# Performance work log

Hardware: AMD Instinct MI355X
Metric: run time of the kernel (lower is better)

Reference implementation:

```python
import jax, jax.numpy as jnp
import numpy as np

B, T, C, H = 2, 2048, 1024, 16
D = C // H  # head dim = 64


def setup_inputs() -> dict:
    key = jax.random.key(0)
    k1, k2, k3 = jax.random.split(key, 3)
    x = jax.random.normal(k1, (B, T, C), dtype=jnp.float32)
    w_attn = jax.random.normal(k2, (C, 3 * C), dtype=jnp.float32) * (1.0 / np.sqrt(C))
    b_attn = jnp.zeros((3 * C,), dtype=jnp.float32)
    w_proj = jax.random.normal(k3, (C, C), dtype=jnp.float32) * (1.0 / np.sqrt(C))
    b_proj = jnp.zeros((C,), dtype=jnp.float32)
    return {"x": x, "w_attn": w_attn, "b_attn": b_attn, "w_proj": w_proj, "b_proj": b_proj}


def reference(x, w_attn, b_attn, w_proj, b_proj):
    Bx, Tx, Cx = x.shape
    qkv = x @ w_attn + b_attn  # [B, T, 3C]
    q, k, v = jnp.split(qkv, 3, axis=-1)
    # [B, H, T, D]
    q = q.reshape(Bx, Tx, H, D).swapaxes(1, 2)
    k = k.reshape(Bx, Tx, H, D).swapaxes(1, 2)
    v = v.reshape(Bx, Tx, H, D).swapaxes(1, 2)
    scale = 1.0 / jnp.sqrt(jnp.float32(D))
    att = jnp.einsum('bhqd,bhkd->bhqk', q, k) * scale  # [B, H, T, T]
    causal = jnp.tril(jnp.ones((Tx, Tx), dtype=bool))
    att = jnp.where(causal[None, None], att, -jnp.inf)
    att = jax.nn.softmax(att, axis=-1)
    y = jnp.einsum('bhqk,bhkd->bhqd', att, v)  # [B, H, T, D]
    y = y.swapaxes(1, 2).reshape(Bx, Tx, Cx)
    return y @ w_proj + b_proj
```

## Files before the change

### kernel.cpp

```cpp
#include <hip/hip_runtime.h>
#include <hip/hip_bf16.h>


typedef __attribute__((ext_vector_type(8))) short short8x;
typedef __attribute__((ext_vector_type(4))) float float4x;
typedef __attribute__((ext_vector_type(4))) unsigned short ushort4x;
typedef __attribute__((ext_vector_type(2))) unsigned int uint2x;

#define MFMA_BF16 __builtin_amdgcn_mfma_f32_16x16x32_bf16

typedef const __attribute__((address_space(1))) void gvoid_t;
typedef __attribute__((address_space(3))) void lvoid_t;
#define GLOAD_LDS16(g, l) __builtin_amdgcn_global_load_lds((gvoid_t*)(g), (lvoid_t*)(l), 16, 0, 0)

__device__ __forceinline__ unsigned short f2b(float f) {
    unsigned int u = __float_as_uint(f);
    u = (u + 0x7FFFu + ((u >> 16) & 1u)) >> 16;
    return (unsigned short)u;
}
__device__ __forceinline__ unsigned int pk2(float a, float b) {
    return __builtin_amdgcn_perm(__float_as_uint(b) + 0x8000u,
                                 __float_as_uint(a) + 0x8000u, 0x07060302u);
}
__device__ __forceinline__ unsigned int pk2t(float a, float b) {
    return __builtin_amdgcn_perm(__float_as_uint(b),
                                 __float_as_uint(a), 0x07060302u);
}

__device__ __forceinline__ void stage32(const unsigned short* g, size_t rs,
                                        short* ldst, int w0, int lane) {
    const int r8 = lane >> 3;
    const int sc = ((lane & 7) ^ r8) * 8;
#pragma unroll
    for (int q = 0; q < 4; q++) {
        GLOAD_LDS16(g + (size_t)(w0 + q * 8 + r8) * rs + sc,
                    ldst + (w0 + q * 8) * 64);
    }
}

__global__ __launch_bounds__(256) void prep(const float* __restrict__ x,
                                            unsigned short* __restrict__ xb,
                                            const float* __restrict__ wa,
                                            unsigned short* __restrict__ waT,
                                            const float* __restrict__ wp,
                                            unsigned short* __restrict__ wpT) {
    __shared__ float tile[32][33];
    const int blk = blockIdx.x;
    if (blk < 4096) {
        int i = blk * 256 + threadIdx.x;
        float4 v = ((const float4*)x)[i];
        ushort4x o = { f2b(v.x), f2b(v.y), f2b(v.z), f2b(v.w) };
        ((ushort4x*)xb)[i] = o;
        return;
    }
    int idx = blk - 4096;
    int bx = idx & 127;
    int by = idx >> 7;
    const float* in;
    unsigned short* outp;
    int cols;
    if (bx < 96) { in = wa; outp = waT; cols = 3072; }
    else         { in = wp; outp = wpT; cols = 1024; bx -= 96; }
    const int tx = threadIdx.x & 31, ty = threadIdx.x >> 5;
    const int cbase = bx * 32, rbase = by * 32;
    int c = cbase + tx;
    for (int j = 0; j < 32; j += 8)
        tile[ty + j][tx] = in[(size_t)(rbase + ty + j) * cols + c];
    __syncthreads();
    int rr = rbase + tx;
    for (int j = 0; j < 32; j += 8) {
        int cc = cbase + ty + j;
        outp[(size_t)cc * 1024 + rr] = f2b(tile[tx][ty + j]);
    }
}

template <bool SWAP>
__device__ __forceinline__ void qkv_mainloop(const unsigned short* Ag,
                                             const unsigned short* Bg,
                                             short* lA, short* lB,
                                             float4x (&acc)[4][4],
                                             int wave, int lane, int wr, int wc,
                                             int quad, int l16, int sw) {
    const int K = 1024;
    for (int kk = 0; kk < K; kk += 64) {
        stage32(Ag + kk, K, lA, wave * 32, lane);
        stage32(Bg + kk, K, lB, wave * 32, lane);
        __syncthreads();

#pragma unroll
        for (int kk2 = 0; kk2 < 2; kk2++) {
            short8x a[4], b[4];
#pragma unroll
            for (int i = 0; i < 4; i++)
                a[i] = *(const short8x*)&lA[(wr * 64 + i * 16 + l16) * 64 +
                                            ((kk2 * 4 + quad) ^ sw) * 8];
#pragma unroll
            for (int j = 0; j < 4; j++)
                b[j] = *(const short8x*)&lB[(wc * 64 + j * 16 + l16) * 64 +
                                            ((kk2 * 4 + quad) ^ sw) * 8];
#pragma unroll
            for (int i = 0; i < 4; i++)
#pragma unroll
                for (int j = 0; j < 4; j++)
                    acc[i][j] = SWAP ? MFMA_BF16(b[j], a[i], acc[i][j], 0, 0, 0)
                                     : MFMA_BF16(a[i], b[j], acc[i][j], 0, 0, 0);
        }
        __syncthreads();
    }
}

__global__ __launch_bounds__(256, 4) void gemm_qkv(const unsigned short* __restrict__ A,
                                                   const unsigned short* __restrict__ BT,
                                                   const float* __restrict__ bias,
                                                   unsigned short* __restrict__ QK,
                                                   unsigned short* __restrict__ VTg) {
    __shared__ union {
        struct { short A[128 * 64]; short B[128 * 64]; } s;
        short vt[4][64 * 80];
    } lds;

    const int K = 1024;
    const int lane = threadIdx.x & 63;
    const int wave = threadIdx.x >> 6;
    const int quad = lane >> 4;
    const int l16  = lane & 15;
    const int sw   = l16 & 7;

    const int rblk = blockIdx.y * 128;
    const int cblk = blockIdx.x * 128;
    const int wr = wave >> 1, wc = wave & 1;
    const bool qk = (blockIdx.x < 16);

    float4x acc[4][4] = {};

    const unsigned short* Ag = A  + (size_t)rblk * K;
    const unsigned short* Bg = BT + (size_t)cblk * K;

    if (qk) qkv_mainloop<true >(Ag, Bg, lds.s.A, lds.s.B, acc, wave, lane, wr, wc, quad, l16, sw);
    else    qkv_mainloop<false>(Ag, Bg, lds.s.A, lds.s.B, acc, wave, lane, wr, wc, quad, l16, sw);

    const int rbase = rblk + wr * 64;
    const int cbase = cblk + wc * 64;

    if (qk) {
        const float sc = (blockIdx.x < 8) ? 0.18033688f : 1.0f;
#pragma unroll
        for (int i = 0; i < 4; i++) {
            const int r = rbase + i * 16 + l16;
#pragma unroll
            for (int j = 0; j < 4; j++) {
                const int c = cbase + j * 16 + quad * 4;
                float4 bv = *(const float4*)&bias[c];
                uint2x p = { pk2((acc[i][j][0] + bv.x) * sc, (acc[i][j][1] + bv.y) * sc),
                             pk2((acc[i][j][2] + bv.z) * sc, (acc[i][j][3] + bv.w) * sc) };
                *(uint2x*)&QK[(size_t)r * 2048 + c] = p;
            }
        }
    } else {
#pragma unroll
        for (int i = 0; i < 4; i++) {
#pragma unroll
            for (int j = 0; j < 4; j++) {
                int c = cbase + j * 16 + l16;
                float bv = bias[c];
                uint2x p = { pk2(acc[i][j][0] + bv, acc[i][j][1] + bv),
                             pk2(acc[i][j][2] + bv, acc[i][j][3] + bv) };
                *(uint2x*)&lds.vt[wave][(j * 16 + l16) * 80 + i * 16 + quad * 4] = p;
            }
        }
        const int h   = (cbase - 2048) >> 6;
        const int hb  = (rbase >> 11) * 16 + h;
        const int tb0 = rbase & 2047;
#pragma unroll
        for (int p = 0; p < 8; p++) {
            int dd   = p * 8 + (lane >> 3);
            int toff = (lane & 7) * 8;
            short8x vv = *(const short8x*)&lds.vt[wave][dd * 80 + toff];
            *(short8x*)&VTg[((size_t)(hb * 64 + dd)) * 2048 + tb0 + toff] = vv;
        }
    }
}

__global__ __launch_bounds__(256) void gemm_proj(const unsigned short* __restrict__ A,
                                                 const unsigned short* __restrict__ BT,
                                                 const float* __restrict__ bias,
                                                 float* __restrict__ out) {
    __shared__ struct { short A[64 * 64]; short B[128 * 64]; } lds;

    const int K = 1024, N = 1024;
    const int lane = threadIdx.x & 63;
    const int wave = threadIdx.x >> 6;
    const int quad = lane >> 4;
    const int l16  = lane & 15;
    const int sw   = l16 & 7;

    const int rblk = blockIdx.y * 64;
    const int cblk = blockIdx.x * 128;

    float4x acc[4][2] = {};

    const unsigned short* Ag = A  + (size_t)rblk * K;
    const unsigned short* Bg = BT + (size_t)cblk * K;

    for (int kk = 0; kk < K; kk += 64) {
        if (wave < 2) {
            stage32(Ag + kk, K, lds.A, wave * 32, lane);
        } else {
            stage32(Bg + kk, K, lds.B, (wave - 2) * 64, lane);
            stage32(Bg + kk, K, lds.B, (wave - 2) * 64 + 32, lane);
        }
        __syncthreads();

#pragma unroll
        for (int kk2 = 0; kk2 < 2; kk2++) {
            short8x b[2];
#pragma unroll
            for (int j = 0; j < 2; j++)
                b[j] = *(const short8x*)&lds.B[(wave * 32 + j * 16 + l16) * 64 +
                                               ((kk2 * 4 + quad) ^ sw) * 8];
#pragma unroll
            for (int i = 0; i < 4; i++) {
                short8x a = *(const short8x*)&lds.A[(i * 16 + l16) * 64 +
                                                    ((kk2 * 4 + quad) ^ sw) * 8];
#pragma unroll
                for (int j = 0; j < 2; j++)
                    acc[i][j] = MFMA_BF16(a, b[j], acc[i][j], 0, 0, 0);
            }
        }
        __syncthreads();
    }

#pragma unroll
    for (int j = 0; j < 2; j++) {
        const int c = cblk + wave * 32 + j * 16 + l16;
        const float bv = bias[c];
#pragma unroll
        for (int i = 0; i < 4; i++) {
#pragma unroll
            for (int reg = 0; reg < 4; reg++) {
                int r = rblk + i * 16 + quad * 4 + reg;
                out[(size_t)r * N + c] = acc[i][j][reg] + bv;
            }
        }
    }
}

__global__ __launch_bounds__(256) void attn_kernel(const unsigned short* __restrict__ QK,
                                                   const unsigned short* __restrict__ VT,
                                                   unsigned short* __restrict__ Y) {
    __shared__ __attribute__((aligned(16))) short Kl[2][64 * 64];
    __shared__ __attribute__((aligned(16))) short Vl[2][64 * 64];
    __shared__ __attribute__((aligned(16))) short Pl[4][2048];

    const int tid  = threadIdx.x;
    const int lane = tid & 63;
    const int wave = tid >> 6;
    const int quad = lane >> 4;
    const int l16  = lane & 15;
    const int sw   = l16 & 7;

    const int bid = blockIdx.x;
    const int qb  = 31 - (bid >> 5);
    const int bh  = bid & 31;
    const int b = bh >> 4, h = bh & 15;

    const unsigned short* Qp = QK + ((size_t)b * 2048) * 2048 + h * 64;
    const unsigned short* Kp = Qp + 1024;
    const unsigned short* Vp = VT + (size_t)bh * 64 * 2048;

    const int qbase = qb * 64 + wave * 16;
    const int ntb   = qb + 1;

    short8x aq[2];
#pragma unroll
    for (int kk = 0; kk < 2; kk++)
        aq[kk] = *(const short8x*)(Qp + (size_t)(qbase + l16) * 2048 + kk * 32 + quad * 8);

    const short ONE = (short)0x3F80;
    const short8x ones = { ONE, ONE, ONE, ONE, ONE, ONE, ONE, ONE };

    if (wave < 2) stage32(Kp, 2048, Kl[0], wave * 32, lane);
    else          stage32(Vp, 2048, Vl[0], (wave - 2) * 32, lane);
    __syncthreads();

    float4x lacc = {};
    float4x O[4] = {};

    for (int it = 0; it < ntb; it++) {
        const int kb = it * 64;
        const short* Kc = Kl[it & 1];
        const short* Vc = Vl[it & 1];

        if (it + 1 < ntb) {
            const int kb2 = kb + 64;
            if (wave < 2) stage32(Kp + (size_t)kb2 * 2048, 2048, Kl[(it + 1) & 1], wave * 32, lane);
            else          stage32(Vp + kb2, 2048, Vl[(it + 1) & 1], (wave - 2) * 32, lane);
        }

        float4x S[4];
#pragma unroll
        for (int t = 0; t < 4; t++) {
            short8x kf0 = *(const short8x*)&Kc[(t * 16 + l16) * 64 + ((quad) ^ sw) * 8];
            short8x kf1 = *(const short8x*)&Kc[(t * 16 + l16) * 64 + ((4 + quad) ^ sw) * 8];
            S[t] = (float4x){0.f, 0.f, 0.f, 0.f};
            S[t] = MFMA_BF16(kf0, aq[0], S[t], 0, 0, 0);
            S[t] = MFMA_BF16(kf1, aq[1], S[t], 0, 0, 0);
        }

        if (kb + 64 > qbase) {
            int q = qbase + l16;
#pragma unroll
            for (int t = 0; t < 4; t++)
#pragma unroll
                for (int reg = 0; reg < 4; reg++)
                    if (kb + t * 16 + quad * 4 + reg > q) S[t][reg] = -1e38f;
        }

#pragma unroll
        for (int t = 0; t < 4; t++) {
            float e0 = __builtin_amdgcn_exp2f(S[t][0]);
            float e1 = __builtin_amdgcn_exp2f(S[t][1]);
            float e2 = __builtin_amdgcn_exp2f(S[t][2]);
            float e3 = __builtin_amdgcn_exp2f(S[t][3]);
            uint2x p = { pk2t(e0, e1), pk2t(e2, e3) };
            *(uint2x*)&Pl[wave][l16 * 64 + ((2 * t + (quad >> 1)) ^ sw) * 8 + (quad & 1) * 4] = p;
        }

#pragma unroll
        for (int kc = 0; kc < 2; kc++) {
            short8x bp = *(const short8x*)&Pl[wave][l16 * 64 + ((4 * kc + quad) ^ sw) * 8];
            lacc = MFMA_BF16(ones, bp, lacc, 0, 0, 0);
#pragma unroll
            for (int dt = 0; dt < 4; dt++) {
                short8x vf = *(const short8x*)&Vc[(dt * 16 + l16) * 64 + ((kc * 4 + quad) ^ sw) * 8];
                O[dt] = MFMA_BF16(vf, bp, O[dt], 0, 0, 0);
            }
        }
        __syncthreads();
    }

    float rl = 1.0f / lacc[0];
#pragma unroll
    for (int dt = 0; dt < 4; dt++) {
        uint2x o = { pk2(O[dt][0] * rl, O[dt][1] * rl),
                     pk2(O[dt][2] * rl, O[dt][3] * rl) };
        *(uint2x*)&Pl[wave][l16 * 64 + ((2 * dt + (quad >> 1)) ^ sw) * 8 + (quad & 1) * 4] = o;
    }
    const int t = qbase + l16;
#pragma unroll
    for (int cc = 0; cc < 2; cc++) {
        short8x row = *(const short8x*)&Pl[wave][l16 * 64 + ((2 * quad + cc) ^ sw) * 8];
        *(short8x*)&Y[((size_t)(b * 2048 + t)) * 1024 + h * 64 + (2 * quad + cc) * 8] = row;
    }
}

extern "C" void kernel_launch(void* const* d_in, const int* in_sizes, int n_in,
                              void* d_out, int out_size, void* d_ws, size_t ws_size,
                              hipStream_t stream) {
    const float* x      = (const float*)d_in[0];
    const float* w_attn = (const float*)d_in[1];
    const float* b_attn = (const float*)d_in[2];
    const float* w_proj = (const float*)d_in[3];
    const float* b_proj = (const float*)d_in[4];
    float* out = (float*)d_out;

    char* ws = (char*)d_ws;
    unsigned short* xb  = (unsigned short*)(ws + (size_t)0);
    unsigned short* waT = (unsigned short*)(ws + (size_t)(8  << 20));
    unsigned short* wpT = (unsigned short*)(ws + (size_t)(14 << 20));
    unsigned short* QKb = (unsigned short*)(ws + (size_t)(16 << 20));
    unsigned short* VTb = (unsigned short*)(ws + (size_t)(32 << 20));
    unsigned short* yb  = (unsigned short*)(ws + (size_t)(40 << 20));

    prep<<<8192, 256, 0, stream>>>(x, xb, w_attn, waT, w_proj, wpT);

    gemm_qkv<<<dim3(24, 32), 256, 0, stream>>>(xb, waT, b_attn, QKb, VTb);

    attn_kernel<<<1024, 256, 0, stream>>>(QKb, VTb, yb);

    gemm_proj<<<dim3(8, 64), 256, 0, stream>>>(yb, wpT, b_proj, out);
}
```

Before: 164.0 us.

## Split long causal attention rows over two KV halves and combine partials

Query blocks 16-31, which have the most causal KV tiles, are each split into two work items covering KV tiles [0,1024) and [1024,end). Each item writes unnormalized fp32 partial O and row-sum L to workspace, and a new combine kernel sums the halves and normalizes to bf16. The grid is reordered so every block has at most 16 tiles, which balances load and shortens the tail. The cost is an extra kernel launch plus partial-result traffic. Summing partials without a max rescale relies on the existing softmax having no running max.

```diff
diff --git a/kernel.cpp b/kernel.cpp
--- a/kernel.cpp
+++ b/kernel.cpp
@@ -247,10 +247,12 @@
 
 __global__ __launch_bounds__(256) void attn_kernel(const unsigned short* __restrict__ QK,
                                                    const unsigned short* __restrict__ VT,
-                                                   unsigned short* __restrict__ Y) {
+                                                   unsigned short* __restrict__ Y,
+                                                   float* __restrict__ pO,
+                                                   float* __restrict__ pL) {
     __shared__ __attribute__((aligned(16))) short Kl[2][64 * 64];
     __shared__ __attribute__((aligned(16))) short Vl[2][64 * 64];
-    __shared__ __attribute__((aligned(16))) short Pl[4][2048];
+    __shared__ __attribute__((aligned(16))) short Pl[4][16 * 64];
 
     const int tid  = threadIdx.x;
     const int lane = tid & 63;
@@ -260,8 +262,22 @@
     const int sw   = l16 & 7;
 
     const int bid = blockIdx.x;
-    const int qb  = 31 - (bid >> 5);
-    const int bh  = bid & 31;
+    int qb, bh, kb0, nt, half;
+    bool split;
+    if (bid < 512) {
+        qb = 16 + (bid >> 5); bh = bid & 31; kb0 = 0;    nt = 16; split = true;  half = 0;
+    } else if (bid < 544) {
+        qb = 15;             bh = bid & 31; kb0 = 0;    nt = 16; split = false; half = 0;
+    } else if (bid < 576) {
+        qb = 31;             bh = bid & 31; kb0 = 1024; nt = 16; split = true;  half = 1;
+    } else {
+        const int g = (bid - 576) >> 6;
+        const int r = (bid - 576) & 63;
+        const int L = 15 - g;
+        bh = r & 31;
+        if (r < 32) { qb = L - 1;  kb0 = 0;    nt = L; split = false; half = 0; }
+        else        { qb = L + 15; kb0 = 1024; nt = L; split = true;  half = 1; }
+    }
     const int b = bh >> 4, h = bh & 15;
 
     const unsigned short* Qp = QK + ((size_t)b * 2048) * 2048 + h * 64;
@@ -269,7 +285,6 @@
     const unsigned short* Vp = VT + (size_t)bh * 64 * 2048;
 
     const int qbase = qb * 64 + wave * 16;
-    const int ntb   = qb + 1;
 
     short8x aq[2];
 #pragma unroll
@@ -279,19 +294,19 @@
     const short ONE = (short)0x3F80;
     const short8x ones = { ONE, ONE, ONE, ONE, ONE, ONE, ONE, ONE };
 
-    if (wave < 2) stage32(Kp, 2048, Kl[0], wave * 32, lane);
-    else          stage32(Vp, 2048, Vl[0], (wave - 2) * 32, lane);
+    if (wave < 2) stage32(Kp + (size_t)kb0 * 2048, 2048, Kl[0], wave * 32, lane);
+    else          stage32(Vp + kb0, 2048, Vl[0], (wave - 2) * 32, lane);
     __syncthreads();
 
     float4x lacc = {};
     float4x O[4] = {};
 
-    for (int it = 0; it < ntb; it++) {
-        const int kb = it * 64;
+    for (int it = 0; it < nt; it++) {
+        const int kb = kb0 + it * 64;
         const short* Kc = Kl[it & 1];
         const short* Vc = Vl[it & 1];
 
-        if (it + 1 < ntb) {
+        if (it + 1 < nt) {
             const int kb2 = kb + 64;
             if (wave < 2) stage32(Kp + (size_t)kb2 * 2048, 2048, Kl[(it + 1) & 1], wave * 32, lane);
             else          stage32(Vp + kb2, 2048, Vl[(it + 1) & 1], (wave - 2) * 32, lane);
@@ -339,6 +354,17 @@
         __syncthreads();
     }
 
+    if (split) {
+        const int pblk = bh * 16 + (qb - 16);
+        const int ql   = wave * 16 + l16;
+        float* po = pO + ((size_t)(pblk * 2 + half)) * 4096;
+#pragma unroll
+        for (int dt = 0; dt < 4; dt++)
+            *(float4x*)&po[ql * 64 + dt * 16 + quad * 4] = O[dt];
+        if (quad == 0) pL[pblk * 128 + half * 64 + ql] = lacc[0];
+        return;
+    }
+
     float rl = 1.0f / lacc[0];
 #pragma unroll
     for (int dt = 0; dt < 4; dt++) {
@@ -351,6 +377,32 @@
     for (int cc = 0; cc < 2; cc++) {
         short8x row = *(const short8x*)&Pl[wave][l16 * 64 + ((2 * quad + cc) ^ sw) * 8];
         *(short8x*)&Y[((size_t)(b * 2048 + t)) * 1024 + h * 64 + (2 * quad + cc) * 8] = row;
+    }
+}
+
+__global__ __launch_bounds__(256) void attn_combine(const float* __restrict__ pO,
+                                                    const float* __restrict__ pL,
+                                                    unsigned short* __restrict__ Y) {
+    const int blk = blockIdx.x;
+    const int bh = blk >> 4;
+    const int qb = 16 + (blk & 15);
+    const int b = bh >> 4, h = bh & 15;
+    const int tid = threadIdx.x;
+    const int q  = tid >> 2;
+    const int c0 = (tid & 3) * 16;
+
+    const float* p0 = pO + ((size_t)blk * 2 + 0) * 4096 + q * 64 + c0;
+    const float* p1 = pO + ((size_t)blk * 2 + 1) * 4096 + q * 64 + c0;
+    const float l = pL[blk * 128 + q] + pL[blk * 128 + 64 + q];
+    const float rl = 1.0f / l;
+    unsigned short* yp = Y + ((size_t)(b * 2048 + qb * 64 + q)) * 1024 + h * 64 + c0;
+#pragma unroll
+    for (int i = 0; i < 4; i++) {
+        float4 a = *(const float4*)(p0 + i * 4);
+        float4 c = *(const float4*)(p1 + i * 4);
+        ushort4x r = { f2b((a.x + c.x) * rl), f2b((a.y + c.y) * rl),
+                       f2b((a.z + c.z) * rl), f2b((a.w + c.w) * rl) };
+        *(ushort4x*)(yp + i * 4) = r;
     }
 }
 
@@ -371,12 +423,16 @@
     unsigned short* QKb = (unsigned short*)(ws + (size_t)(16 << 20));
     unsigned short* VTb = (unsigned short*)(ws + (size_t)(32 << 20));
     unsigned short* yb  = (unsigned short*)(ws + (size_t)(40 << 20));
+    float*          pO  = (float*)(ws + (size_t)(48 << 20));
+    float*          pL  = (float*)(ws + (size_t)(64 << 20));
 
     prep<<<8192, 256, 0, stream>>>(x, xb, w_attn, waT, w_proj, wpT);
 
     gemm_qkv<<<dim3(24, 32), 256, 0, stream>>>(xb, waT, b_attn, QKb, VTb);
 
-    attn_kernel<<<1024, 256, 0, stream>>>(QKb, VTb, yb);
+    attn_kernel<<<1536, 256, 0, stream>>>(QKb, VTb, yb, pO, pL);
+
+    attn_combine<<<512, 256, 0, stream>>>(pO, pL, yb);
 
     gemm_proj<<<dim3(8, 64), 256, 0, stream>>>(yb, wpT, b_proj, out);
 }
```

Result: slower. 170.1 us (+3.8%).
